# Kernel optimization log

Hardware: AMD Instinct MI355X
Metric: run time of the kernel (lower is better)

Reference implementation:

```python
import jax, jax.numpy as jnp
import numpy as np

N_QUBIT = 22
N_LAYERS = 2
D_LOGICAL = 2  # num_logical_dim (one logical qubit)
DIM = 2 ** N_QUBIT


def _apply_ry(psi, th, q):
    # psi: (B, 2^n) complex64; Ry(th) on qubit q (q=0 is the most significant bit)
    half = th * 0.5
    c = jnp.cos(half).astype(jnp.complex64)
    s = jnp.sin(half).astype(jnp.complex64)
    psi4 = psi.reshape(psi.shape[0], 2 ** q, 2, -1)
    p0, p1 = psi4[:, :, 0], psi4[:, :, 1]
    out = jnp.stack([c * p0 - s * p1, s * p0 + c * p1], axis=2)
    return out.reshape(psi.shape)


def _apply_cnot(psi, c, t):
    a, b = (c, t) if c < t else (t, c)
    right = 2 ** (N_QUBIT - b - 1)
    mid = 2 ** (b - a - 1)
    psi6 = psi.reshape(psi.shape[0], 2 ** a, 2, mid, 2, right)
    if c < t:
        # control is axis 2; flip target axis 4 where control==1
        psi6 = psi6.at[:, :, 1, :, :, :].set(psi6[:, :, 1, :, ::-1, :])
    else:
        # control is axis 4; flip target axis 2 where control==1
        psi6 = psi6.at[:, :, :, :, 1, :].set(psi6[:, :, ::-1, :, 1, :])
    return psi6.reshape(psi.shape)


def _apply_pauli(psi, p, q):
    psi4 = psi.reshape(psi.shape[0], 2 ** q, 2, -1)
    p0, p1 = psi4[:, :, 0], psi4[:, :, 1]
    if p == 'X':
        out = jnp.stack([p1, p0], axis=2)
    elif p == 'Y':
        out = jnp.stack([-1j * p1, 1j * p0], axis=2)
    else:  # Z
        out = jnp.stack([p0, -p1], axis=2)
    return out.reshape(psi.shape)


def _encode(theta):
    # q0[i, i] = 1 for the logical basis states, then run the circuit
    psi = jnp.zeros((D_LOGICAL, DIM), jnp.complex64)
    psi = psi.at[jnp.arange(D_LOGICAL), jnp.arange(D_LOGICAL)].set(1.0)
    for l in range(N_LAYERS):
        for q in range(N_QUBIT):
            psi = _apply_ry(psi, theta[l, q], q)
        for q in range(N_QUBIT):
            psi = _apply_cnot(psi, q, (q + 1) % N_QUBIT)
    return psi


def _kl_loss(theta):
    psi = _encode(theta)  # (D_LOGICAL, 2^n)
    # Knill-Laflamme inner products T_e[i,j] = <psi_i| E_e |psi_j> for all weight-1 Paulis
    Ts = []
    for q in range(N_QUBIT):
        for p in ('X', 'Y', 'Z'):
            epsi = _apply_pauli(psi, p, q)
            Ts.append(jnp.einsum('is,js->ij', psi.conj(), epsi))
    T = jnp.stack(Ts)  # (3*N_QUBIT, D_LOGICAL, D_LOGICAL)
    diag = jnp.diagonal(T, axis1=1, axis2=2)
    lam = diag.mean(axis=1)  # per-error lambda_e
    res = T - lam[:, None, None] * jnp.eye(D_LOGICAL, dtype=T.dtype)
    # loss_type == 'L2'
    return jnp.sum(jnp.abs(res) ** 2)


def setup_inputs() -> dict:
    key = jax.random.key(0)
    theta = jax.random.normal(key, (N_LAYERS, N_QUBIT), dtype=jnp.float32)
    return {"theta": theta}


def reference(theta):
    return _kl_loss(theta)
```

## Files before the change

kernel.cpp:

```cpp
#include <hip/hip_runtime.h>

#define NQ 22
#define DIMN (1u << NQ)

struct MaskSet {
    unsigned L[NQ];
    unsigned Linv[NQ];
    unsigned xm[NQ];
    unsigned zm[NQ];
    unsigned frowHi[5];
};

constexpr MaskSet buildMasks() {
    MaskSet M{};
    for (int b = 0; b < NQ; ++b) M.L[b] = 1u << b;
    for (int q = 0; q < NQ; ++q) {
        int bc = NQ - 1 - q, bt = NQ - 1 - ((q + 1) % NQ);
        M.L[bt] ^= M.L[bc];
    }
    unsigned mat[NQ] = {}, aug[NQ] = {};
    for (int b = 0; b < NQ; ++b) { mat[b] = M.L[b]; aug[b] = 1u << b; }
    for (int col = 0; col < NQ; ++col) {
        int piv = col;
        while (!((mat[piv] >> col) & 1u)) ++piv;
        unsigned tm = mat[piv]; mat[piv] = mat[col]; mat[col] = tm;
        unsigned ta = aug[piv]; aug[piv] = aug[col]; aug[col] = ta;
        for (int r = 0; r < NQ; ++r)
            if (r != col && ((mat[r] >> col) & 1u)) { mat[r] ^= mat[col]; aug[r] ^= aug[col]; }
    }
    for (int b = 0; b < NQ; ++b) M.Linv[b] = aug[b];
    for (int j = 0; j < NQ; ++j) {
        int b = NQ - 1 - j;
        unsigned xmv = 0;
        for (int r = 0; r < NQ; ++r)
            if ((aug[r] >> b) & 1u) xmv |= 1u << r;
        M.xm[j] = xmv;
        M.zm[j] = M.L[b];
    }
    for (int j = 0; j < 5; ++j) {
        unsigned f = 0;
        for (int r = 0; r < NQ; ++r)
            if ((aug[r] >> (17 + j)) & 1u) f |= 1u << r;
        M.frowHi[j] = f;
    }
    return M;
}
constexpr int topbit_c(unsigned v) { int b = 0; while (v >> (b + 1)) ++b; return b; }
constexpr unsigned unionHi() {
    MaskSet M = buildMasks();
    unsigned u = 0;
    for (int j = 0; j < 5; ++j) u |= M.frowHi[j];
    return u;
}
static_assert((unionHi() & 0xFFFFu) == 0, "frowHi must only touch bits 16..21");

constexpr unsigned orbGen(int which) {
    MaskSet M = buildMasks();
    return (which == 0 ? M.xm[0] : which == 1 ? M.xm[4] : M.xm[9]) >> 2;
}
constexpr int orbS21() {
    MaskSet M = buildMasks();
    unsigned GA = M.xm[0] >> 2, GB = M.xm[4] >> 2, GC = M.xm[9] >> 2;
    unsigned GQ = M.xm[21] >> 2;
    for (int s = 1; s < 8; ++s) {
        unsigned c = ((s & 1) ? GA : 0u) ^ ((s & 2) ? GB : 0u) ^ ((s & 4) ? GC : 0u);
        if (c == GQ) return s;
    }
    return -1;
}
constexpr bool orbitOK() {
    unsigned GA = orbGen(0), GB = orbGen(1), GC = orbGen(2);
    int cA = topbit_c(GA), cB = topbit_c(GB), cC = topbit_c(GC);
    if (!(cC < cB && cB < cA) || cA > 19) return false;
    if (((GA >> cB) & 1u) || ((GA >> cC) & 1u)) return false;
    if (((GB >> cA) & 1u) || ((GB >> cC) & 1u)) return false;
    if (((GC >> cA) & 1u) || ((GC >> cB) & 1u)) return false;
    return orbS21() > 0;
}
static_assert(orbitOK(), "orbit structure for fused slice measurement must hold");

constexpr bool lowPlanOK() {
    MaskSet M = buildMasks();
    if ((M.xm[10] & ~0xE00u) != 0) return false;
    if ((M.xm[11] & ~0xE00u) != 0) return false;
    for (int q = 12; q <= 19; ++q) {
        if ((M.xm[q] & 3u) != 0 && (M.xm[q] & 3u) != 2u) return false;
        if ((M.zm[q] & 3u) != 0) return false;
        if (topbit_c(M.xm[q]) < 2 || topbit_c(M.xm[q]) > 9) return false;
    }
    if (M.xm[20] != 3u) return false;
    if ((M.zm[20] & 3u) != 2u) return false;
    return true;
}
static_assert(lowPlanOK(), "k_low measurement plan must hold");

__device__ __forceinline__ float fflip(float v, unsigned sbit31) {
    return __int_as_float(__float_as_int(v) ^ (int)sbit31);
}
__device__ __forceinline__ unsigned ph4(unsigned g) { return g ^ ((g >> 6) & 3u); }

__device__ __forceinline__ unsigned sA(unsigned i) {
    return i ^ ((i >> 3) & 7u) ^ (((i >> 6) & 3u) << 3);
}

__device__ __forceinline__ float fold4(float a, float b, float c, float d, int lane) {
    bool p0 = (lane & 1) != 0;
    float kL = p0 ? b : a, sL = p0 ? a : b;
    kL += __shfl_xor(sL, 1);
    float kH = p0 ? d : c, sH = p0 ? c : d;
    kH += __shfl_xor(sH, 1);
    bool p1 = (lane & 2) != 0;
    float k2 = p1 ? kH : kL, s2 = p1 ? kL : kH;
    k2 += __shfl_xor(s2, 2);
    k2 += __shfl_xor(k2, 4);
    k2 += __shfl_xor(k2, 8);
    k2 += __shfl_xor(k2, 16);
    k2 += __shfl_xor(k2, 32);
    return k2;
}

__device__ __forceinline__ void gates3(float* a, float* b, const float* __restrict__ trig, int b0) {
#pragma unroll
    for (int g = 0; g < 3; ++g) {
        float c = trig[2 * NQ + b0 + g], s = trig[3 * NQ + b0 + g];
#pragma unroll
        for (int e = 0; e < 8; ++e) {
            if (!(e & (1 << g))) {
                int e1 = e | (1 << g);
                float x0 = a[e], x1 = a[e1];
                a[e] = c * x0 - s * x1; a[e1] = s * x0 + c * x1;
                float y0 = b[e], y1 = b[e1];
                b[e] = c * y0 - s * y1; b[e1] = s * y0 + c * y1;
            }
        }
    }
}

__global__ __launch_bounds__(256) void k_prep(const float* __restrict__ theta,
                                              float* __restrict__ acc,
                                              float* __restrict__ trig) {
    int t = threadIdx.x;
    acc[t] = 0.f;
    if (t < 2 * NQ) {
        int l = t / NQ, q = t % NQ, b = NQ - 1 - q;
        float h = 0.5f * theta[t];
        trig[l * 2 * NQ + b]      = cosf(h);
        trig[l * 2 * NQ + NQ + b] = sinf(h);
    }
}

__global__ __launch_bounds__(256, 1) void k_genHi(float* __restrict__ phi,
                                                  const float* __restrict__ trig,
                                                  float* __restrict__ acc) {
    constexpr MaskSet M = buildMasks();
    __shared__ float red[4 * 12];
    unsigned base = blockIdx.x * 256u + threadIdx.x;
    unsigned P0 = 0;
#pragma unroll
    for (int b = 0; b < NQ; ++b)
        P0 |= ((unsigned)__popc(base & M.Linv[b]) & 1u) << b;
    float pc = 1.f;
#pragma unroll
    for (int b = 1; b < 16; ++b) {
        float cvb = trig[b], svb = trig[NQ + b];
        pc *= ((P0 >> b) & 1u) ? svb : cvb;
    }
    float cv0 = trig[0], sv0 = trig[NQ];
    float C0 = pc * ((P0 & 1u) ? sv0 : cv0);
    float C1 = pc * ((P0 & 1u) ? cv0 : -sv0);
    float cb[6], sb[6];
#pragma unroll
    for (int k = 0; k < 6; ++k) { cb[k] = trig[16 + k]; sb[k] = trig[NQ + 16 + k]; }
    unsigned u0 = P0 >> 16;
    float v0[32], v1[32];
#pragma unroll
    for (int e = 0; e < 32; ++e) {
        unsigned F = 0;
        if (e & 1)  F ^= M.frowHi[0];
        if (e & 2)  F ^= M.frowHi[1];
        if (e & 4)  F ^= M.frowHi[2];
        if (e & 8)  F ^= M.frowHi[3];
        if (e & 16) F ^= M.frowHi[4];
        unsigned u = u0 ^ (F >> 16);
        float vp = (u & 1u) ? sb[0] : cb[0];
#pragma unroll
        for (int k = 1; k < 6; ++k) vp *= ((u >> k) & 1u) ? sb[k] : cb[k];
        v0[e] = vp * C0;
        v1[e] = vp * C1;
    }
    float c2[5], s2[5];
#pragma unroll
    for (int j = 0; j < 5; ++j) {
        c2[j] = trig[2 * NQ + 17 + j];
        s2[j] = trig[3 * NQ + 17 + j];
    }
#pragma unroll
    for (int j = 0; j < 5; ++j) {
#pragma unroll
        for (int e = 0; e < 32; ++e) {
            if (!(e & (1 << j))) {
                int e1 = e | (1 << j);
                float a0 = v0[e], a1 = v0[e1];
                v0[e]  = c2[j] * a0 - s2[j] * a1;
                v0[e1] = s2[j] * a0 + c2[j] * a1;
                float b0 = v1[e], b1 = v1[e1];
                v1[e]  = c2[j] * b0 - s2[j] * b1;
                v1[e1] = s2[j] * b0 + c2[j] * b1;
            }
        }
    }
#pragma unroll
    for (int e = 0; e < 32; ++e) {
        unsigned a = base | ((unsigned)e << 17);
        phi[a] = v0[e];
        phi[DIMN + a] = v1[e];
    }
    int lane = threadIdx.x & 63, w = threadIdx.x >> 6;
#pragma unroll
    for (int i = 1; i <= 3; ++i) {
        unsigned ex  = M.xm[i] >> 17;
        unsigned zme = M.zm[i] >> 17;
        float t00 = 0.f, t11 = 0.f, t01 = 0.f, u01 = 0.f;
#pragma unroll
        for (int e = 0; e < 32; ++e) {
            int ep = e ^ (int)ex;
            t00 += v0[e] * v0[ep];
            t11 += v1[e] * v1[ep];
            float p = v0[e] * v1[ep];
            t01 += p;
            unsigned sg = ((unsigned)__popc((unsigned)ep & zme) & 1u) << 31;
            u01 += fflip(p, sg);
        }
        float r = fold4(t00, t11, t01, u01, lane);
        if (lane < 4) red[w * 12 + (i - 1) * 4 + lane] = r;
    }
    __syncthreads();
    int t = threadIdx.x;
    if (t < 12) {
        float r = red[t] + red[12 + t] + red[24 + t] + red[36 + t];
        atomicAdd(&acc[4 + t], r);
    }
}

__global__ __launch_bounds__(256, 1) void k_midA(float* __restrict__ phi,
                                                 const float* __restrict__ trig,
                                                 float* __restrict__ acc) {
    constexpr MaskSet M = buildMasks();
    __shared__ float red[4 * 16];
    unsigned tid = blockIdx.x * 256u + threadIdx.x;
    unsigned base = (tid & 0xFFFu) | ((tid >> 12) << 17);
    float v0[32], v1[32];
#pragma unroll
    for (int e = 0; e < 32; ++e) {
        unsigned a = base | ((unsigned)e << 12);
        v0[e] = phi[a];
        v1[e] = phi[DIMN + a];
    }
    float c[5], s[5];
#pragma unroll
    for (int j = 0; j < 5; ++j) {
        c[j] = trig[2 * NQ + 12 + j];
        s[j] = trig[3 * NQ + 12 + j];
    }
#pragma unroll
    for (int j = 0; j < 5; ++j) {
#pragma unroll
        for (int e = 0; e < 32; ++e) {
            if (!(e & (1 << j))) {
                int e1 = e | (1 << j);
                float a0 = v0[e], a1 = v0[e1];
                v0[e]  = c[j] * a0 - s[j] * a1;
                v0[e1] = s[j] * a0 + c[j] * a1;
                float b0 = v1[e], b1 = v1[e1];
                v1[e]  = c[j] * b0 - s[j] * b1;
                v1[e1] = s[j] * b0 + c[j] * b1;
            }
        }
    }
#pragma unroll
    for (int e = 0; e < 32; ++e) {
        unsigned a = base | ((unsigned)e << 12);
        phi[a] = v0[e];
        phi[DIMN + a] = v1[e];
    }
    int lane = threadIdx.x & 63, w = threadIdx.x >> 6;
#pragma unroll
    for (int i = 5; i <= 8; ++i) {
        unsigned ex  = (M.xm[i] >> 12) & 31u;
        unsigned zme = (M.zm[i] >> 12) & 31u;
        unsigned bs31 = ((unsigned)__popc(base & M.zm[i]) & 1u) << 31;
        float t00 = 0.f, t11 = 0.f, t01 = 0.f, u01 = 0.f;
#pragma unroll
        for (int e = 0; e < 32; ++e) {
            int ep = e ^ (int)ex;
            t00 += v0[e] * v0[ep];
            t11 += v1[e] * v1[ep];
            float p = v0[e] * v1[ep];
            t01 += p;
            unsigned sg = ((unsigned)__popc((unsigned)ep & zme) & 1u) << 31;
            u01 += fflip(p, sg ^ bs31);
        }
        float r = fold4(t00, t11, t01, u01, lane);
        if (lane < 4) red[w * 16 + (i - 5) * 4 + lane] = r;
    }
    __syncthreads();
    int t = threadIdx.x;
    if (t < 16) {
        float r = red[t] + red[16 + t] + red[32 + t] + red[48 + t];
        atomicAdd(&acc[20 + t], r);
    }
}

__global__ __launch_bounds__(512, 8) void k_low(float* __restrict__ phi,
                                                const float* __restrict__ trig,
                                                float* __restrict__ acc) {
    constexpr MaskSet M = buildMasks();
    __shared__ float As[4096];
    __shared__ float Bs[4096];
    __shared__ float redZ[8 * 33];
    __shared__ float redQ[8 * 44];
    float4* As4 = (float4*)As;
    float4* Bs4 = (float4*)Bs;
    int t = threadIdx.x;
    int lane = t & 63, w = t >> 6;
    unsigned base = blockIdx.x * 4096u;
    float a[8], b[8];

    {
        const float4* g0 = (const float4*)(phi + base);
        const float4* g1 = (const float4*)(phi + DIMN + base);
#pragma unroll
        for (int k = 0; k < 2; ++k) {
            float4 va = g0[2 * t + k];
            a[4 * k] = va.x; a[4 * k + 1] = va.y; a[4 * k + 2] = va.z; a[4 * k + 3] = va.w;
            float4 vb = g1[2 * t + k];
            b[4 * k] = vb.x; b[4 * k + 1] = vb.y; b[4 * k + 2] = vb.z; b[4 * k + 3] = vb.w;
        }
        gates3(a, b, trig, 0);
#pragma unroll
        for (int j = 0; j < 8; ++j) {
            unsigned i = ((unsigned)t << 3) | (unsigned)j;
            unsigned A = sA(i);
            As[A] = a[j]; Bs[A] = b[j];
        }
    }
    __syncthreads();

    {
#pragma unroll
        for (int j = 0; j < 8; ++j) {
            unsigned i = (((unsigned)t >> 3) << 6) | ((unsigned)j << 3) | ((unsigned)t & 7u);
            unsigned A = sA(i);
            a[j] = As[A]; b[j] = Bs[A];
        }
        gates3(a, b, trig, 3);
#pragma unroll
        for (int j = 0; j < 8; ++j) {
            unsigned i = (((unsigned)t >> 3) << 6) | ((unsigned)j << 3) | ((unsigned)t & 7u);
            unsigned A = sA(i);
            As[A] = a[j]; Bs[A] = b[j];
        }
    }
    __syncthreads();

    {
#pragma unroll
        for (int j = 0; j < 8; ++j) {
            unsigned i = (((unsigned)t >> 6) << 9) | ((unsigned)j << 6) | ((unsigned)t & 63u);
            unsigned A = sA(i);
            a[j] = As[A]; b[j] = Bs[A];
        }
        gates3(a, b, trig, 6);
#pragma unroll
        for (int j = 0; j < 8; ++j) {
            unsigned i = (((unsigned)t >> 6) << 9) | ((unsigned)j << 6) | ((unsigned)t & 63u);
            unsigned A = sA(i);
            As[A] = a[j]; Bs[A] = b[j];
        }
    }
    __syncthreads();

    {
#pragma unroll
        for (int j = 0; j < 8; ++j) {
            unsigned i = ((unsigned)j << 9) | (unsigned)t;
            unsigned A = sA(i);
            a[j] = As[A]; b[j] = Bs[A];
        }
        gates3(a, b, trig, 9);
    }
    __syncthreads();

#pragma unroll
    for (int j = 0; j < 8; ++j) {
        unsigned i = ((unsigned)j << 9) | (unsigned)t;
        phi[base + i] = a[j];
        phi[DIMN + base + i] = b[j];
        unsigned p = i ^ (((i >> 8) & 3u) << 2);
        As[p] = a[j]; Bs[p] = b[j];
    }

#pragma unroll
    for (int c = 0; c < 3; ++c) {
        float p[8];
#pragma unroll
        for (int j = 0; j < 8; ++j)
            p[j] = (c == 0) ? a[j] * a[j] : (c == 1) ? b[j] * b[j] : a[j] * b[j];
        float s1[4], d1[4];
#pragma unroll
        for (int j = 0; j < 4; ++j) { s1[j] = p[j] + p[j + 4]; d1[j] = p[j] - p[j + 4]; }
        float s2_0 = s1[0] + s1[2], s2_1 = s1[1] + s1[3];
        float d2_0 = d1[0] - d1[2], d2_1 = d1[1] - d1[3];
        float SS = s2_0 + s2_1;
        float z0 = (d1[0] + d1[1]) + (d1[2] + d1[3]);
        float z1 = d2_0 + d2_1;
        float d3 = d2_0 - d2_1;
        float r = fold4(SS, z0, z1, 0.f, lane);
        if (lane < 3) redZ[w * 33 + c * 11 + lane] = r;
        float v = d3;
#pragma unroll
        for (int s = 0; s < 6; ++s) {
            float u = __shfl_xor(v, 1 << s);
            v = u + fflip(v, ((unsigned)(lane >> s) & 1u) << 31);
        }
        int pcnt = __popc(lane);
        if (lane == 64 - (64 >> pcnt)) redZ[w * 33 + c * 11 + 3 + pcnt] = v;
    }
    __syncthreads();

    if (t < 66) {
        int c = t % 3, q = t / 3;
        int idx, wm;
        if (q == 0 || q == 21)      { idx = 9; wm = 7; }
        else if (q <= 9)            { idx = 0; wm = 0; }
        else if (q == 10)           { idx = 1; wm = 0; }
        else if (q == 11)           { idx = 2; wm = 0; }
        else if (q == 12)           { idx = 3; wm = 0; }
        else if (q == 13)           { idx = 3; wm = 4; }
        else if (q == 14)           { idx = 3; wm = 6; }
        else if (q == 15)           { idx = 3; wm = 7; }
        else                        { idx = q - 12; wm = 7; }
        float val = 0.f;
#pragma unroll
        for (int ww = 0; ww < 8; ++ww) {
            float rv = redZ[ww * 33 + c * 11 + idx];
            val += ((__popc(ww & wm) & 1) ? -rv : rv);
        }
        unsigned sg = (unsigned)__popc(base & M.zm[q]) & 1u;
        atomicAdd(&acc[4 * NQ + 3 * q + c], sg ? -val : val);
    }

#pragma unroll
    for (int i = 0; i < 2; ++i) {
        int q = 10 + i;
        unsigned je  = (M.xm[q] >> 9) & 7u;
        unsigned zmj = (M.zm[q] >> 9) & 7u;
        unsigned zb31 = ((unsigned)__popc(base & M.zm[q]) & 1u) << 31;
        float t00 = 0.f, t11 = 0.f, t01 = 0.f, u01 = 0.f;
#pragma unroll
        for (int j = 0; j < 8; ++j) {
            int jp = j ^ (int)je;
            t00 += a[j] * a[jp];
            t11 += b[j] * b[jp];
            float p = a[j] * b[jp];
            t01 += p;
            unsigned sg = ((unsigned)__popc((unsigned)jp & zmj) & 1u) << 31;
            u01 += fflip(p, sg ^ zb31);
        }
        float r = fold4(t00, t11, t01, u01, lane);
        if (lane < 4) redQ[w * 44 + 4 * i + lane] = r;
    }

#pragma unroll
    for (int iq = 2; iq < 10; ++iq) {
        int q = 10 + iq;
        unsigned m = M.xm[q], zm = M.zm[q];
        unsigned zb = (unsigned)__popc(base & zm) & 1u;
        int gb = topbit_c(M.xm[q]) - 2;
        unsigned mg4 = m >> 2;
        unsigned swap2 = m & 3u;
        float t00 = 0.f, t11 = 0.f, t01 = 0.f, u01 = 0.f;
        unsigned gc = (unsigned)t;
        unsigned g = ((gc >> gb) << (gb + 1)) | (gc & ((1u << gb) - 1u));
        unsigned gx = g ^ mg4;
        float4 a0 = As4[ph4(g)],  a1 = Bs4[ph4(g)];
        float4 b0 = As4[ph4(gx)], b1 = Bs4[ph4(gx)];
        if (swap2) {
            b0 = make_float4(b0.z, b0.w, b0.x, b0.y);
            b1 = make_float4(b1.z, b1.w, b1.x, b1.y);
        }
        unsigned szg = ((unsigned)__popc((g << 2) & zm) + zb) & 1u;
        unsigned szx = ((unsigned)__popc((gx << 2) & zm) + zb) & 1u;
        unsigned fg = szg << 31, fx = szx << 31;
        const float* A0 = &a0.x; const float* A1 = &a1.x;
        const float* B0 = &b0.x; const float* B1 = &b1.x;
#pragma unroll
        for (int j = 0; j < 4; ++j) {
            t00 += A0[j] * B0[j];
            t11 += A1[j] * B1[j];
            float p = A0[j] * B1[j], r2 = B0[j] * A1[j];
            t01 += p + r2;
            u01 += fflip(p, fx) + fflip(r2, fg);
        }
        t00 *= 2.f; t11 *= 2.f;
        float r = fold4(t00, t11, t01, u01, lane);
        if (lane < 4) redQ[w * 44 + 4 * iq + lane] = r;
    }
    {
        unsigned zm = M.zm[20];
        unsigned zb = (unsigned)__popc(base & zm) & 1u;
        float t00 = 0.f, t11 = 0.f, t01 = 0.f, u01 = 0.f;
#pragma unroll
        for (int k = 0; k < 2; ++k) {
            unsigned g = (unsigned)t + 512u * k;
            float4 a0 = As4[ph4(g)], a1 = Bs4[ph4(g)];
            unsigned szg = ((unsigned)__popc((g << 2) & zm) + zb) & 1u;
            const float* A0 = &a0.x; const float* A1 = &a1.x;
#pragma unroll
            for (int j = 0; j < 4; ++j) {
                int jx = j ^ 3;
                float p = A0[j] * A0[jx];
                float q2 = A1[j] * A1[jx];
                float cr = A0[j] * A1[jx];
                t00 += p; t11 += q2; t01 += cr;
                unsigned sj = ((unsigned)(jx >> 1) & 1u) ^ szg;
                u01 += fflip(cr, sj << 31);
            }
        }
        float r = fold4(t00, t11, t01, u01, lane);
        if (lane < 4) redQ[w * 44 + 40 + lane] = r;
    }
    __syncthreads();
    if (t < 44) {
        float r = 0.f;
#pragma unroll
        for (int ww = 0; ww < 8; ++ww) r += redQ[ww * 44 + t];
        atomicAdd(&acc[40 + t], r);
    }
}

__global__ __launch_bounds__(256) void k_measF(const float* __restrict__ phi,
                                               float* __restrict__ acc) {
    constexpr MaskSet M = buildMasks();
    constexpr unsigned GA = orbGen(0), GB = orbGen(1), GC = orbGen(2);
    constexpr int pc0 = topbit_c(GC), pc1 = topbit_c(GB), pc2 = topbit_c(GA);
    __shared__ float red[4 * 16];
    unsigned t = blockIdx.x * 256u + threadIdx.x;
    unsigned g = t;
    g = ((g >> pc0) << (pc0 + 1)) | (g & ((1u << pc0) - 1u));
    g = ((g >> pc1) << (pc1 + 1)) | (g & ((1u << pc1) - 1u));
    g = ((g >> pc2) << (pc2 + 1)) | (g & ((1u << pc2) - 1u));
    const float4* P0 = (const float4*)phi;
    const float4* P1 = (const float4*)(phi + DIMN);
    unsigned idx[8];
    float4 u4[8], w4[8];
#pragma unroll
    for (int s = 0; s < 8; ++s) {
        idx[s] = g ^ ((s & 1) ? GA : 0u) ^ ((s & 2) ? GB : 0u) ^ ((s & 4) ? GC : 0u);
        u4[s] = P0[idx[s]];
        w4[s] = P1[idx[s]];
    }
    constexpr int QN[4] = { 0, 4, 9, 21 };
    constexpr int SX[4] = { 1, 2, 4, orbS21() };
    float res[16];
#pragma unroll
    for (int qi = 0; qi < 4; ++qi) {
        const unsigned xq = M.xm[QN[qi]];
        const unsigned zq = M.zm[QN[qi]];
        const int sx = SX[qi];
        const int mu = (int)(xq & 3u);
        const unsigned zh = zq >> 2, zl = zq & 3u;
        unsigned fz[8];
#pragma unroll
        for (int s = 0; s < 8; ++s)
            fz[s] = ((unsigned)__popc(idx[s] & zh) & 1u) << 31;
        unsigned pj31[4];
#pragma unroll
        for (int j = 0; j < 4; ++j)
            pj31[j] = ((unsigned)__popc((unsigned)j & zl) & 1u) << 31;
        float t00 = 0.f, t11 = 0.f, t01 = 0.f, u01 = 0.f;
#pragma unroll
        for (int s = 0; s < 8; ++s) {
            const int s2 = s ^ sx;
            const float* A0 = &u4[s].x;
            const float* A1 = &w4[s].x;
            const float* B0 = &u4[s2].x;
            const float* B1 = &w4[s2].x;
            const unsigned fe = fz[s2];
#pragma unroll
            for (int j = 0; j < 4; ++j) {
                const int jp = j ^ mu;
                t00 += A0[j] * B0[jp];
                t11 += A1[j] * B1[jp];
                float p = A0[j] * B1[jp];
                t01 += p;
                u01 += fflip(p, fe ^ pj31[jp]);
            }
        }
        res[4 * qi + 0] = t00; res[4 * qi + 1] = t11;
        res[4 * qi + 2] = t01; res[4 * qi + 3] = u01;
    }
    int lane = threadIdx.x & 63, w = threadIdx.x >> 6;
#pragma unroll
    for (int g4 = 0; g4 < 4; ++g4) {
        float r = fold4(res[4 * g4 + 0], res[4 * g4 + 1], res[4 * g4 + 2], res[4 * g4 + 3], lane);
        if (lane < 4) red[w * 16 + 4 * g4 + lane] = r;
    }
    __syncthreads();
    int tt = threadIdx.x;
    if (tt < 16) {
        int qi = tt >> 2;
        int base4 = (qi == 0) ? 0 : (qi == 1) ? 16 : (qi == 2) ? 36 : 84;
        float r = red[tt] + red[16 + tt] + red[32 + tt] + red[48 + tt];
        atomicAdd(&acc[base4 + (tt & 3)], r);
    }
}

__global__ __launch_bounds__(64) void k_final(const float* __restrict__ acc,
                                              float* __restrict__ out) {
    int t = threadIdx.x;
    float v = 0.f;
    if (t < NQ) {
        float t00 = acc[4 * t], t11 = acc[4 * t + 1];
        float t01 = acc[4 * t + 2], u01 = acc[4 * t + 3];
        float d = t00 - t11;
        v = 0.5f * d * d + 2.f * t01 * t01 + 2.f * u01 * u01;
    } else if (t < 2 * NQ) {
        int q = t - NQ;
        float z0 = acc[4 * NQ + 3 * q], z1 = acc[4 * NQ + 3 * q + 1];
        float zz = acc[4 * NQ + 3 * q + 2];
        float d = z0 - z1;
        v = 0.5f * d * d + 2.f * zz * zz;
    }
    v += __shfl_down(v, 32); v += __shfl_down(v, 16); v += __shfl_down(v, 8);
    v += __shfl_down(v, 4);  v += __shfl_down(v, 2);  v += __shfl_down(v, 1);
    if (t == 0) out[0] = v;
}

extern "C" void kernel_launch(void* const* d_in, const int* in_sizes, int n_in,
                              void* d_out, int out_size, void* d_ws, size_t ws_size,
                              hipStream_t stream) {
    const float* theta = (const float*)d_in[0];
    float* out  = (float*)d_out;
    float* ws   = (float*)d_ws;
    float* phi  = ws;
    float* acc  = ws + 2 * (size_t)DIMN;
    float* trig = acc + 256;

    k_prep<<<1, 256, 0, stream>>>(theta, acc, trig);
    k_genHi<<<512, 256, 0, stream>>>(phi, trig, acc);
    k_midA<<<512, 256, 0, stream>>>(phi, trig, acc);
    k_low<<<1024, 512, 0, stream>>>(phi, trig, acc);
    k_measF<<<512, 256, 0, stream>>>(phi, acc);
    k_final<<<1, 64, 0, stream>>>(acc, out);
}
```

Measured before the change: 156.3 us.

## Drop prep and final kernels; use per-block partials with last-block reduction

Removes the k_prep and k_final launches. Each kernel now computes the Ry cos/sin table itself into shared memory, and every block writes its partial sums to a workspace slot instead of issuing atomicAdds. The last block of k_measF, detected through a threadfence plus an atomic counter, sums all partials and evaluates the loss. This trades two launches and atomic contention for redundant trig work per block and a serial tail reduction in one block. k_low's occupancy hint also drops from 8 to 4 blocks per CU.

```diff
diff --git a/kernel.cpp b/kernel.cpp
--- a/kernel.cpp
+++ b/kernel.cpp
@@ -2,6 +2,12 @@
 
 #define NQ 22
 #define DIMN (1u << NQ)
+
+#define PG_OFF 0u
+#define PM_OFF 6144u
+#define PL_OFF 14336u
+#define PF_OFF 126976u
+#define CNT_OFF 135168u
 
 struct MaskSet {
     unsigned L[NQ];
@@ -119,7 +125,16 @@
     return k2;
 }
 
-__device__ __forceinline__ void gates3(float* a, float* b, const float* __restrict__ trig, int b0) {
+__device__ __forceinline__ void buildTrig(float* trig, const float* __restrict__ theta, int t) {
+    if (t < 2 * NQ) {
+        int l = t / NQ, q = t % NQ, b = NQ - 1 - q;
+        float h = 0.5f * theta[t];
+        trig[l * 2 * NQ + b]      = cosf(h);
+        trig[l * 2 * NQ + NQ + b] = sinf(h);
+    }
+}
+
+__device__ __forceinline__ void gates3(float* a, float* b, const float* trig, int b0) {
 #pragma unroll
     for (int g = 0; g < 3; ++g) {
         float c = trig[2 * NQ + b0 + g], s = trig[3 * NQ + b0 + g];
@@ -136,24 +151,15 @@
     }
 }
 
-__global__ __launch_bounds__(256) void k_prep(const float* __restrict__ theta,
-                                              float* __restrict__ acc,
-                                              float* __restrict__ trig) {
-    int t = threadIdx.x;
-    acc[t] = 0.f;
-    if (t < 2 * NQ) {
-        int l = t / NQ, q = t % NQ, b = NQ - 1 - q;
-        float h = 0.5f * theta[t];
-        trig[l * 2 * NQ + b]      = cosf(h);
-        trig[l * 2 * NQ + NQ + b] = sinf(h);
-    }
-}
-
 __global__ __launch_bounds__(256, 1) void k_genHi(float* __restrict__ phi,
-                                                  const float* __restrict__ trig,
-                                                  float* __restrict__ acc) {
+                                                  const float* __restrict__ theta,
+                                                  float* __restrict__ P) {
     constexpr MaskSet M = buildMasks();
     __shared__ float red[4 * 12];
+    __shared__ float trig[4 * NQ];
+    if (blockIdx.x == 0 && threadIdx.x == 0) *(int*)(P + CNT_OFF) = 0;
+    buildTrig(trig, theta, threadIdx.x);
+    __syncthreads();
     unsigned base = blockIdx.x * 256u + threadIdx.x;
     unsigned P0 = 0;
 #pragma unroll
@@ -238,15 +244,18 @@
     int t = threadIdx.x;
     if (t < 12) {
         float r = red[t] + red[12 + t] + red[24 + t] + red[36 + t];
-        atomicAdd(&acc[4 + t], r);
+        P[PG_OFF + (unsigned)t * 512u + blockIdx.x] = r;
     }
 }
 
 __global__ __launch_bounds__(256, 1) void k_midA(float* __restrict__ phi,
-                                                 const float* __restrict__ trig,
-                                                 float* __restrict__ acc) {
+                                                 const float* __restrict__ theta,
+                                                 float* __restrict__ P) {
     constexpr MaskSet M = buildMasks();
     __shared__ float red[4 * 16];
+    __shared__ float trig[4 * NQ];
+    buildTrig(trig, theta, threadIdx.x);
+    __syncthreads();
     unsigned tid = blockIdx.x * 256u + threadIdx.x;
     unsigned base = (tid & 0xFFFu) | ((tid >> 12) << 17);
     float v0[32], v1[32];
@@ -307,35 +316,37 @@
     int t = threadIdx.x;
     if (t < 16) {
         float r = red[t] + red[16 + t] + red[32 + t] + red[48 + t];
-        atomicAdd(&acc[20 + t], r);
-    }
-}
-
-__global__ __launch_bounds__(512, 8) void k_low(float* __restrict__ phi,
-                                                const float* __restrict__ trig,
-                                                float* __restrict__ acc) {
+        P[PM_OFF + (unsigned)t * 512u + blockIdx.x] = r;
+    }
+}
+
+__global__ __launch_bounds__(512, 4) void k_low(float* __restrict__ phi,
+                                                const float* __restrict__ theta,
+                                                float* __restrict__ P) {
     constexpr MaskSet M = buildMasks();
     __shared__ float As[4096];
     __shared__ float Bs[4096];
     __shared__ float redZ[8 * 33];
     __shared__ float redQ[8 * 44];
+    __shared__ float trig[4 * NQ];
     float4* As4 = (float4*)As;
     float4* Bs4 = (float4*)Bs;
     int t = threadIdx.x;
     int lane = t & 63, w = t >> 6;
     unsigned base = blockIdx.x * 4096u;
     float a[8], b[8];
+    buildTrig(trig, theta, t);
 
     {
         const float4* g0 = (const float4*)(phi + base);
         const float4* g1 = (const float4*)(phi + DIMN + base);
-#pragma unroll
-        for (int k = 0; k < 2; ++k) {
-            float4 va = g0[2 * t + k];
-            a[4 * k] = va.x; a[4 * k + 1] = va.y; a[4 * k + 2] = va.z; a[4 * k + 3] = va.w;
-            float4 vb = g1[2 * t + k];
-            b[4 * k] = vb.x; b[4 * k + 1] = vb.y; b[4 * k + 2] = vb.z; b[4 * k + 3] = vb.w;
-        }
+        float4 va0 = g0[2 * t], va1 = g0[2 * t + 1];
+        float4 vb0 = g1[2 * t], vb1 = g1[2 * t + 1];
+        a[0] = va0.x; a[1] = va0.y; a[2] = va0.z; a[3] = va0.w;
+        a[4] = va1.x; a[5] = va1.y; a[6] = va1.z; a[7] = va1.w;
+        b[0] = vb0.x; b[1] = vb0.y; b[2] = vb0.z; b[3] = vb0.w;
+        b[4] = vb1.x; b[5] = vb1.y; b[6] = vb1.z; b[7] = vb1.w;
+        __syncthreads();
         gates3(a, b, trig, 0);
 #pragma unroll
         for (int j = 0; j < 8; ++j) {
@@ -447,7 +458,7 @@
             val += ((__popc(ww & wm) & 1) ? -rv : rv);
         }
         unsigned sg = (unsigned)__popc(base & M.zm[q]) & 1u;
-        atomicAdd(&acc[4 * NQ + 3 * q + c], sg ? -val : val);
+        P[PL_OFF + (44u + (unsigned)t) * 1024u + blockIdx.x] = sg ? -val : val;
     }
 
 #pragma unroll
@@ -535,16 +546,19 @@
         float r = 0.f;
 #pragma unroll
         for (int ww = 0; ww < 8; ++ww) r += redQ[ww * 44 + t];
-        atomicAdd(&acc[40 + t], r);
+        P[PL_OFF + (unsigned)t * 1024u + blockIdx.x] = r;
     }
 }
 
 __global__ __launch_bounds__(256) void k_measF(const float* __restrict__ phi,
-                                               float* __restrict__ acc) {
+                                               float* __restrict__ P,
+                                               float* __restrict__ out) {
     constexpr MaskSet M = buildMasks();
     constexpr unsigned GA = orbGen(0), GB = orbGen(1), GC = orbGen(2);
     constexpr int pc0 = topbit_c(GC), pc1 = topbit_c(GB), pc2 = topbit_c(GA);
     __shared__ float red[4 * 16];
+    __shared__ float accv[160];
+    __shared__ int lastBlk;
     unsigned t = blockIdx.x * 256u + threadIdx.x;
     unsigned g = t;
     g = ((g >> pc0) << (pc0 + 1)) | (g & ((1u << pc0) - 1u));
@@ -609,32 +623,56 @@
     __syncthreads();
     int tt = threadIdx.x;
     if (tt < 16) {
-        int qi = tt >> 2;
-        int base4 = (qi == 0) ? 0 : (qi == 1) ? 16 : (qi == 2) ? 36 : 84;
         float r = red[tt] + red[16 + tt] + red[32 + tt] + red[48 + tt];
-        atomicAdd(&acc[base4 + (tt & 3)], r);
-    }
-}
-
-__global__ __launch_bounds__(64) void k_final(const float* __restrict__ acc,
-                                              float* __restrict__ out) {
-    int t = threadIdx.x;
+        P[PF_OFF + (unsigned)tt * 512u + blockIdx.x] = r;
+    }
+    __threadfence();
+    __syncthreads();
+    if (tt == 0) {
+        int c = atomicAdd((int*)(P + CNT_OFF), 1);
+        lastBlk = (c == (int)gridDim.x - 1);
+    }
+    __syncthreads();
+    if (!lastBlk) return;
+    __threadfence();
+    if (tt < 154) {
+        const float* rb; int n; int slot;
+        if (tt < 12)       { rb = P + PG_OFF + (unsigned)tt * 512u;        n = 512;  slot = 4 + tt; }
+        else if (tt < 28)  { rb = P + PM_OFF + (unsigned)(tt - 12) * 512u; n = 512;  slot = 20 + (tt - 12); }
+        else if (tt < 72)  { rb = P + PL_OFF + (unsigned)(tt - 28) * 1024u; n = 1024; slot = 40 + (tt - 28); }
+        else if (tt < 138) { rb = P + PL_OFF + (unsigned)(tt - 28) * 1024u; n = 1024; slot = 88 + (tt - 72); }
+        else {
+            int j = tt - 138;
+            rb = P + PF_OFF + (unsigned)j * 512u; n = 512;
+            int qi = j >> 2;
+            int b4 = (qi == 0) ? 0 : (qi == 1) ? 16 : (qi == 2) ? 36 : 84;
+            slot = b4 + (j & 3);
+        }
+        const float4* r4 = (const float4*)rb;
+        float S = 0.f;
+        for (int i = 0; i < n / 4; ++i) {
+            float4 x = r4[i];
+            S += (x.x + x.y) + (x.z + x.w);
+        }
+        accv[slot] = S;
+    }
+    __syncthreads();
     float v = 0.f;
-    if (t < NQ) {
-        float t00 = acc[4 * t], t11 = acc[4 * t + 1];
-        float t01 = acc[4 * t + 2], u01 = acc[4 * t + 3];
+    if (tt < NQ) {
+        float t00 = accv[4 * tt], t11 = accv[4 * tt + 1];
+        float t01 = accv[4 * tt + 2], u01 = accv[4 * tt + 3];
         float d = t00 - t11;
         v = 0.5f * d * d + 2.f * t01 * t01 + 2.f * u01 * u01;
-    } else if (t < 2 * NQ) {
-        int q = t - NQ;
-        float z0 = acc[4 * NQ + 3 * q], z1 = acc[4 * NQ + 3 * q + 1];
-        float zz = acc[4 * NQ + 3 * q + 2];
+    } else if (tt < 2 * NQ) {
+        int q = tt - NQ;
+        float z0 = accv[88 + 3 * q], z1 = accv[88 + 3 * q + 1];
+        float zz = accv[88 + 3 * q + 2];
         float d = z0 - z1;
         v = 0.5f * d * d + 2.f * zz * zz;
     }
     v += __shfl_down(v, 32); v += __shfl_down(v, 16); v += __shfl_down(v, 8);
     v += __shfl_down(v, 4);  v += __shfl_down(v, 2);  v += __shfl_down(v, 1);
-    if (t == 0) out[0] = v;
+    if (tt == 0) out[0] = v;
 }
 
 extern "C" void kernel_launch(void* const* d_in, const int* in_sizes, int n_in,
@@ -644,13 +682,10 @@
     float* out  = (float*)d_out;
     float* ws   = (float*)d_ws;
     float* phi  = ws;
-    float* acc  = ws + 2 * (size_t)DIMN;
-    float* trig = acc + 256;
-
-    k_prep<<<1, 256, 0, stream>>>(theta, acc, trig);
-    k_genHi<<<512, 256, 0, stream>>>(phi, trig, acc);
-    k_midA<<<512, 256, 0, stream>>>(phi, trig, acc);
-    k_low<<<1024, 512, 0, stream>>>(phi, trig, acc);
-    k_measF<<<512, 256, 0, stream>>>(phi, acc);
-    k_final<<<1, 64, 0, stream>>>(acc, out);
-}
+    float* P    = ws + 2 * (size_t)DIMN;
+
+    k_genHi<<<512, 256, 0, stream>>>(phi, theta, P);
+    k_midA<<<512, 256, 0, stream>>>(phi, theta, P);
+    k_low<<<1024, 512, 0, stream>>>(phi, theta, P);
+    k_measF<<<512, 256, 0, stream>>>(phi, P, out);
+}
```

Result: slower. 195.3 us (+25.0%).
